# Optimization experiments

Hardware: AMD Instinct MI355X
Metric: run time of the kernel (lower is better)

The kernel has to match this reference:

```python
import jax, jax.numpy as jnp
import numpy as np

B, N, DIM = 1, 32768, 512
H, DH = 8, 64            # heads, dim_head
INNER = H * DH           # 512
L = 64                   # n_cluster = clip(N // (16*16) + 1, 16, 64) = 64 landmarks
ITERS = 6                # pinv_iterations
KS = 33                  # residual_conv_kernel


def setup_inputs() -> dict:
    key = jax.random.key(0)
    k1, k2, k3, k4, k5 = jax.random.split(key, 5)
    x = jax.random.normal(k1, (B, N, DIM), jnp.float32)
    labels = jax.random.randint(k2, (N,), 0, L, jnp.int32)  # kmeans cluster ids (no_grad constants)
    Wqkv = jax.random.normal(k3, (DIM, 3 * INNER), jnp.float32) * 0.02
    Wout = jax.random.normal(k4, (INNER, DIM), jnp.float32) * 0.02
    bout = jnp.zeros((DIM,), jnp.float32)
    res_kernel = jax.random.normal(k5, (H, 1, KS, 1), jnp.float32) * 0.05  # depthwise conv, groups=H
    return dict(x=x, Wqkv=Wqkv, Wout=Wout, bout=bout, res_kernel=res_kernel, labels=labels)


def _pinv(a, iters=ITERS):
    # Moore-Penrose via Newton-Schulz, matching moore_penrose_iter_pinv (global max normalization)
    abs_a = jnp.abs(a)
    z = a.swapaxes(-1, -2) / (abs_a.sum(-1).max() * abs_a.sum(-2).max())
    I = jnp.eye(a.shape[-1], dtype=a.dtype)
    for _ in range(iters):
        az = a @ z
        z = 0.25 * z @ (13.0 * I - az @ (15.0 * I - az @ (7.0 * I - az)))
    return z


def _pool_mean(t, seg):
    # ragged per-cluster mean: t [b,h,n,d], seg [n] sorted cluster ids -> [b,h,L,d]
    b, h, n, d = t.shape
    flat = t.transpose(2, 0, 1, 3).reshape(n, b * h * d)
    sums = jax.ops.segment_sum(flat, seg, num_segments=L)
    counts = jax.ops.segment_sum(jnp.ones((n,), t.dtype), seg, num_segments=L)
    means = sums / jnp.maximum(counts, 1.0)[:, None]
    return means.reshape(L, b, h, d).transpose(1, 2, 0, 3)


def reference(x, Wqkv, Wout, bout, res_kernel, labels):
    # cluster sort / unsort (mirrors x[:, index] ... out[:, index_ori])
    index = jnp.argsort(labels)
    index_ori = jnp.argsort(index)
    seg = labels[index]                      # sorted segment ids
    xp = x[:, index]

    qkv = xp @ Wqkv                          # [b,n,3*inner]
    q, k, v = jnp.split(qkv, 3, axis=-1)
    to_bhnd = lambda t: t.reshape(B, N, H, DH).transpose(0, 2, 1, 3)
    q, k, v = to_bhnd(q), to_bhnd(k), to_bhnd(v)

    ql = _pool_mean(q, seg)                  # [b,h,L,d]
    kl = _pool_mean(k, seg)

    # note: original forward never multiplies by self.scale
    attn1 = jax.nn.softmax(jnp.einsum('bhnd,bhld->bhnl', q, kl), axis=-1)   # [b,h,n,L]
    attn2 = jax.nn.softmax(jnp.einsum('bhid,bhjd->bhij', ql, kl), axis=-1)  # [b,h,L,L]
    attn3 = jax.nn.softmax(jnp.einsum('bhld,bhnd->bhln', ql, k), axis=-1)   # [b,h,L,n]

    out = attn1 @ (_pinv(attn2) @ (attn3 @ v))                              # [b,h,n,d]

    # residual depthwise conv over token axis (Conv2d(h,h,(33,1),groups=h))
    res = jax.lax.conv_general_dilated(
        v, res_kernel, window_strides=(1, 1),
        padding=((KS // 2, KS // 2), (0, 0)),
        dimension_numbers=('NCHW', 'OIHW', 'NCHW'),
        feature_group_count=H)
    out = out + res

    out = out.transpose(0, 2, 1, 3).reshape(B, N, INNER)
    out = out @ Wout + bout
    return out[:, index_ori]
```

## Files before the change

kernel.cpp:

```cpp
#include <hip/hip_runtime.h>
#include <hip/hip_bf16.h>

#define N_TOK 32768
#define DIMC  512
#define NH    8
#define DHD   64
#define NL    64
#define KSZ   33
#define QKVC  1536
#define NCHUNK 64

typedef _Float16 f16;
typedef _Float16 f16x8 __attribute__((ext_vector_type(8)));
typedef _Float16 f16x4 __attribute__((ext_vector_type(4)));
typedef float    f32x4 __attribute__((ext_vector_type(4)));

#define GLOAD_LDS16(gp, lp) \
    __builtin_amdgcn_global_load_lds((const __attribute__((address_space(1))) void*)(gp), \
                                     (__attribute__((address_space(3))) void*)(lp), 16, 0, 0)

__global__ void transpose_k(const float* __restrict__ W, f16* __restrict__ WT, int R, int C) {
    __shared__ float tile[32][33];
    int bx = blockIdx.x * 32, by = blockIdx.y * 32;
    int tx = threadIdx.x, ty = threadIdx.y;
    #pragma unroll
    for (int i = 0; i < 32; i += 8)
        tile[ty + i][tx] = W[(size_t)(by + ty + i) * C + bx + tx];
    __syncthreads();
    #pragma unroll
    for (int i = 0; i < 32; i += 8)
        WT[(size_t)(bx + ty + i) * R + by + tx] = (f16)tile[tx][ty + i];
}

__global__ void hist_k(const int* __restrict__ labels, int* __restrict__ counts) {
    __shared__ int hloc[NL];
    int t = threadIdx.x;
    if (t < NL) hloc[t] = 0;
    __syncthreads();
    int i = blockIdx.x * 256 + t;
    atomicAdd(&hloc[labels[i]], 1);
    __syncthreads();
    if (t < NL) atomicAdd(&counts[t], hloc[t]);
}

__global__ __launch_bounds__(256) void compact_k(const int* __restrict__ labels,
                                                 const int* __restrict__ counts,
                                                 int* __restrict__ indexArr) {
    const int l = blockIdx.x;
    __shared__ int wtot[4];
    __shared__ int s_run;
    int t = threadIdx.x, lane = t & 63, w = t >> 6;
    if (t == 0) {
        int s = 0;
        for (int j = 0; j < l; ++j) s += counts[j];
        s_run = s;
    }
    __syncthreads();
    for (int c0 = 0; c0 < N_TOK; c0 += 256) {
        int ii = c0 + t;
        bool flag = (labels[ii] == l);
        unsigned long long mask = __ballot(flag);
        int before = __popcll(mask & ((1ull << lane) - 1ull));
        if (lane == 0) wtot[w] = __popcll(mask);
        __syncthreads();
        int off = 0;
        #pragma unroll
        for (int ww = 0; ww < 4; ++ww) off += (ww < w) ? wtot[ww] : 0;
        int tot = wtot[0] + wtot[1] + wtot[2] + wtot[3];
        int rb = s_run;
        if (flag) indexArr[rb + off + before] = ii;
        __syncthreads();
        if (t == 0) s_run = rb + tot;
    }
}

__global__ __launch_bounds__(256) void gather_cvt_k(const float4* __restrict__ x4,
                                                    const int* __restrict__ indexArr,
                                                    f16x4* __restrict__ xh4) {
    int t = threadIdx.x;
    int row = blockIdx.x * 2 + (t >> 7);
    int c4 = t & 127;
    int j = indexArr[row];
    float4 v = x4[(size_t)j * 128 + c4];
    f16x4 o = { (f16)v.x, (f16)v.y, (f16)v.z, (f16)v.w };
    xh4[(size_t)row * 128 + c4] = o;
}

template<int BNTOT, bool OUT_F32, int NY>
__global__ __launch_bounds__(512, 4) void gemm_k512(const f16* __restrict__ A, const f16* __restrict__ BT,
                                                    void* __restrict__ Cout, const float* __restrict__ bias,
                                                    const int* __restrict__ scatterIdx) {
    constexpr int K = 512;
    constexpr int NKT = K / 32;
    __shared__ f16 As[3][128 * 32];
    __shared__ f16 Bs[3][256 * 32];
    const int t = threadIdx.x;
    const int orig = blockIdx.x + gridDim.x * blockIdx.y;
    constexpr int NWG = 256 * NY;
    constexpr int CPX = NWG / 8;
    const int lin = (orig & 7) * CPX + (orig >> 3);
    const int mBase = (lin / NY) * 128;
    const int nBase = (lin % NY) * 256;
    const int w = t >> 6, lane = t & 63;
    const int wm = w >> 2, wn = w & 3;
    const int lr = lane & 15, lk = lane >> 4;
    const int kc = (lk ^ ((lr >> 1) & 3)) * 8;
    f32x4 acc[4][4];
    #pragma unroll
    for (int m = 0; m < 4; ++m)
        #pragma unroll
        for (int n = 0; n < 4; ++n) acc[m][n] = (f32x4){0.f, 0.f, 0.f, 0.f};

    auto stage = [&](int buf, int kt) {
        {
            int id = t;
            int row = id >> 2, c = id & 3;
            int cg = c ^ ((row >> 1) & 3);
            GLOAD_LDS16(&A[(size_t)(mBase + row) * K + kt * 32 + cg * 8],
                        &As[buf][(size_t)(w * 64) * 8]);
        }
        #pragma unroll
        for (int r = 0; r < 2; ++r) {
            int id = r * 512 + t;
            int row = id >> 2, c = id & 3;
            int cg = c ^ ((row >> 1) & 3);
            GLOAD_LDS16(&BT[(size_t)(nBase + row) * K + kt * 32 + cg * 8],
                        &Bs[buf][(size_t)(r * 512 + w * 64) * 8]);
        }
    };
    auto compute = [&](int buf) {
        f16x8 af[4], bf[4];
        #pragma unroll
        for (int m = 0; m < 4; ++m)
            af[m] = *(const f16x8*)&As[buf][(wm * 64 + m * 16 + lr) * 32 + kc];
        #pragma unroll
        for (int n = 0; n < 4; ++n)
            bf[n] = *(const f16x8*)&Bs[buf][(wn * 64 + n * 16 + lr) * 32 + kc];
        #pragma unroll
        for (int m = 0; m < 4; ++m)
            #pragma unroll
            for (int n = 0; n < 4; ++n)
                acc[m][n] = __builtin_amdgcn_mfma_f32_16x16x32_f16(bf[n], af[m], acc[m][n], 0, 0, 0);
    };

    stage(0, 0);
    asm volatile("" ::: "memory");
    stage(1, 1);
    for (int kt = 0; kt < NKT; ++kt) {
        if (kt < NKT - 1) {
            asm volatile("s_waitcnt vmcnt(3)" ::: "memory");
        } else {
            asm volatile("s_waitcnt vmcnt(0)" ::: "memory");
        }
        __builtin_amdgcn_s_barrier();
        if (kt + 2 < NKT) stage((kt + 2) % 3, kt + 2);
        compute(kt % 3);
    }

    #pragma unroll
    for (int m = 0; m < 4; ++m) {
        int row = mBase + wm * 64 + m * 16 + lr;
        int srow = OUT_F32 ? scatterIdx[row] : row;
        #pragma unroll
        for (int n = 0; n < 4; ++n) {
            int col = nBase + wn * 64 + n * 16 + lk * 4;
            if constexpr (OUT_F32) {
                float4 bv = *(const float4*)&bias[col];
                float4 sv = make_float4(acc[m][n][0] + bv.x, acc[m][n][1] + bv.y,
                                        acc[m][n][2] + bv.z, acc[m][n][3] + bv.w);
                *(float4*)&((float*)Cout)[(size_t)srow * BNTOT + col] = sv;
            } else {
                f16x4 hv = { (f16)acc[m][n][0], (f16)acc[m][n][1],
                             (f16)acc[m][n][2], (f16)acc[m][n][3] };
                *(f16x4*)&((f16*)Cout)[(size_t)srow * BNTOT + col] = hv;
            }
        }
    }
}

__global__ __launch_bounds__(256) void pool_part_k(const f16* __restrict__ qkvh,
                                                   const int* __restrict__ counts,
                                                   float* __restrict__ psum) {
    int l = blockIdx.x, g = blockIdx.y;
    int t = threadIdx.x;
    int c = t & 127, rg = t >> 7;
    int b0 = 0;
    for (int j = 0; j < l; ++j) b0 += counts[j];
    int cnt = counts[l];
    f32x4 a0 = {0.f,0.f,0.f,0.f}, a1 = {0.f,0.f,0.f,0.f};
    for (int p = g * 2 + rg; p < cnt; p += 8) {
        f16x8 v = *(const f16x8*)&qkvh[(size_t)(b0 + p) * QKVC + c * 8];
        a0[0] += (float)v[0]; a0[1] += (float)v[1]; a0[2] += (float)v[2]; a0[3] += (float)v[3];
        a1[0] += (float)v[4]; a1[1] += (float)v[5]; a1[2] += (float)v[6]; a1[3] += (float)v[7];
    }
    __shared__ f32x4 red[2][128][2];
    red[rg][c][0] = a0; red[rg][c][1] = a1;
    __syncthreads();
    if (t < 128) {
        f32x4 s0 = red[0][t][0] + red[1][t][0];
        f32x4 s1 = red[0][t][1] + red[1][t][1];
        size_t o = ((size_t)g * NL + l) * 1024 + t * 8;
        *(f32x4*)&psum[o] = s0;
        *(f32x4*)&psum[o + 4] = s1;
    }
}

__global__ __launch_bounds__(256) void pool_fin_k(const float* __restrict__ psum,
                                                  const int* __restrict__ counts,
                                                  float* __restrict__ ql, float* __restrict__ kl,
                                                  f16* __restrict__ qlh, f16* __restrict__ klh) {
    int l = blockIdx.x;
    int t = threadIdx.x;
    int bse = t * 4;
    float inv = 1.0f / (float)(counts[l] > 0 ? counts[l] : 1);
    f32x4 s = {0.f,0.f,0.f,0.f};
    #pragma unroll
    for (int g = 0; g < 4; ++g)
        s += *(const f32x4*)&psum[((size_t)g * NL + l) * 1024 + bse];
    s *= inv;
    f16x4 hv = { (f16)s[0], (f16)s[1], (f16)s[2], (f16)s[3] };
    if (bse < 512) {
        int h = bse >> 6, d0 = bse & 63;
        size_t o = ((size_t)(h * 64 + l)) * 64 + d0;
        *(f32x4*)&ql[o] = s;
        *(f16x4*)&qlh[o] = hv;
    } else {
        int bb = bse - 512;
        int h = bb >> 6, d0 = bb & 63;
        size_t o = ((size_t)(h * 64 + l)) * 64 + d0;
        *(f32x4*)&kl[o] = s;
        *(f16x4*)&klh[o] = hv;
    }
}

__global__ __launch_bounds__(256) void attn2_k(const float* __restrict__ ql, const float* __restrict__ kl,
                                               float* __restrict__ a_out, float* __restrict__ mrow,
                                               float* __restrict__ mcol) {
    int h = blockIdx.x;
    __shared__ float qs[64][65], ks[64][65], a[64][65];
    __shared__ float red[64][4];
    __shared__ float rowv[64], colv[64];
    int t = threadIdx.x;
    for (int idx = t; idx < 4096; idx += 256) {
        int r = idx >> 6, c = idx & 63;
        qs[r][c] = ql[h * 4096 + idx];
        ks[r][c] = kl[h * 4096 + idx];
    }
    __syncthreads();
    int i = t >> 2, q4 = t & 3, j0 = q4 * 16;
    float o[16];
    #pragma unroll
    for (int jj = 0; jj < 16; ++jj) o[jj] = 0.f;
    for (int d = 0; d < 64; ++d) {
        float qv = qs[i][d];
        #pragma unroll
        for (int jj = 0; jj < 16; ++jj) o[jj] += qv * ks[j0 + jj][d];
    }
    float pmx = o[0];
    #pragma unroll
    for (int jj = 1; jj < 16; ++jj) pmx = fmaxf(pmx, o[jj]);
    red[i][q4] = pmx;
    __syncthreads();
    float rm = fmaxf(fmaxf(red[i][0], red[i][1]), fmaxf(red[i][2], red[i][3]));
    float psum = 0.f;
    #pragma unroll
    for (int jj = 0; jj < 16; ++jj) { o[jj] = expf(o[jj] - rm); psum += o[jj]; }
    __syncthreads();
    red[i][q4] = psum;
    __syncthreads();
    float rs = red[i][0] + red[i][1] + red[i][2] + red[i][3];
    float inv = 1.0f / rs;
    #pragma unroll
    for (int jj = 0; jj < 16; ++jj) { o[jj] *= inv; a[i][j0 + jj] = o[jj]; }
    __syncthreads();
    for (int idx = t; idx < 4096; idx += 256) a_out[h * 4096 + idx] = a[idx >> 6][idx & 63];
    float rsum = 0.f;
    #pragma unroll
    for (int jj = 0; jj < 16; ++jj) rsum += o[jj];
    __syncthreads();
    red[i][q4] = rsum;
    __syncthreads();
    if (q4 == 0) rowv[i] = red[i][0] + red[i][1] + red[i][2] + red[i][3];
    float csum = 0.f;
    #pragma unroll
    for (int jj = 0; jj < 16; ++jj) csum += a[j0 + jj][i];
    __syncthreads();
    red[i][q4] = csum;
    __syncthreads();
    if (q4 == 0) colv[i] = red[i][0] + red[i][1] + red[i][2] + red[i][3];
    __syncthreads();
    if (t == 0) {
        float mr = rowv[0], mc = colv[0];
        for (int j = 1; j < 64; ++j) { mr = fmaxf(mr, rowv[j]); mc = fmaxf(mc, colv[j]); }
        mrow[h] = mr; mcol[h] = mc;
    }
}

__global__ __launch_bounds__(256) void attn3_pinv_k(const f16* __restrict__ qkvh,
                                                    const f16* __restrict__ qlh,
                                                    float* __restrict__ pm, float* __restrict__ ps,
                                                    float* __restrict__ pacc,
                                                    const float* __restrict__ a_g,
                                                    const float* __restrict__ mrow,
                                                    const float* __restrict__ mcol,
                                                    float* __restrict__ zg) {
    union ShU {
        struct { f16 Qls[64 * 64]; f16 Ks[64 * 64]; f16 vT[64 * 72]; f16 Ps[64 * 72]; float fsh[64]; } a3;
        struct { f16 zRh[64][72], zRl[64][72], cRh[64][72], cRl[64][72],
                 Xh[64][72], Xl[64][72], Yh[64][72], Yl[64][72]; } pv;
    };
    __shared__ ShU sh;
    const int t = threadIdx.x;
    const int w = t >> 6, lane = t & 63;
    const int lr = lane & 15;
    const int h = blockIdx.y;

    if (blockIdx.x == 0) {
        const int lk = lane >> 4;
        f16 (&zRh)[64][72] = sh.pv.zRh; f16 (&zRl)[64][72] = sh.pv.zRl;
        f16 (&cRh)[64][72] = sh.pv.cRh; f16 (&cRl)[64][72] = sh.pv.cRl;
        f16 (&Xh)[64][72]  = sh.pv.Xh;  f16 (&Xl)[64][72]  = sh.pv.Xl;
        f16 (&Yh)[64][72]  = sh.pv.Yh;  f16 (&Yl)[64][72]  = sh.pv.Yl;
        float mr = mrow[0], mc = mcol[0];
        #pragma unroll
        for (int k = 1; k < 8; ++k) { mr = fmaxf(mr, mrow[k]); mc = fmaxf(mc, mcol[k]); }
        const float inv0 = 1.0f / (mr * mc);
        for (int idx = t; idx < 4096; idx += 256) {
            int r = idx >> 6, c = idx & 63;
            float zv = a_g[h * 4096 + idx] * inv0;
            f16 hv = (f16)zv;
            zRh[c][r] = hv; zRl[c][r] = (f16)(zv - (float)hv);
        }
        __syncthreads();

        f32x4 po[4];
        auto product = [&](const f16 (*Lh)[72], const f16 (*Ll)[72],
                           const f16 (*Rh)[72], const f16 (*Rl)[72]) {
            #pragma unroll
            for (int n = 0; n < 4; ++n) po[n] = (f32x4){0.f, 0.f, 0.f, 0.f};
            #pragma unroll
            for (int ck = 0; ck < 2; ++ck) {
                f16x8 axh = *(const f16x8*)&Lh[w * 16 + lr][ck * 32 + lk * 8];
                f16x8 axl = *(const f16x8*)&Ll[w * 16 + lr][ck * 32 + lk * 8];
                #pragma unroll
                for (int n = 0; n < 4; ++n) {
                    f16x8 byh = *(const f16x8*)&Rh[n * 16 + lr][ck * 32 + lk * 8];
                    f16x8 byl = *(const f16x8*)&Rl[n * 16 + lr][ck * 32 + lk * 8];
                    po[n] = __builtin_amdgcn_mfma_f32_16x16x32_f16(byh, axh, po[n], 0, 0, 0);
                    po[n] = __builtin_amdgcn_mfma_f32_16x16x32_f16(byl, axh, po[n], 0, 0, 0);
                    po[n] = __builtin_amdgcn_mfma_f32_16x16x32_f16(byh, axl, po[n], 0, 0, 0);
                }
            }
        };

        for (int it = 0; it < 6; ++it) {
            for (int idx = t; idx < 4096; idx += 256) {
                int r = idx >> 6, c = idx & 63;
                float av = a_g[h * 4096 + idx];
                f16 ah = (f16)av;
                Xh[r][c] = ah; Xl[r][c] = (f16)(av - (float)ah);
                float zv = (float)zRh[r][c] + (float)zRl[r][c];
                f16 zh = (f16)zv;
                Yh[c][r] = zh; Yl[c][r] = (f16)(zv - (float)zh);
            }
            __syncthreads();
            product(Xh, Xl, Yh, Yl);
            __syncthreads();
            #pragma unroll
            for (int n = 0; n < 4; ++n)
                #pragma unroll
                for (int j = 0; j < 4; ++j) {
                    int r = w * 16 + lr, c = n * 16 + lk * 4 + j;
                    float v = po[n][j]; f16 hv = (f16)v; f16 lv = (f16)(v - (float)hv);
                    cRh[r][c] = hv; cRl[r][c] = lv;
                    Xh[c][r] = hv;  Xl[c][r] = lv;
                }
            __syncthreads();
            product(cRh, cRl, Xh, Xl);
            #pragma unroll
            for (int n = 0; n < 4; ++n)
                #pragma unroll
                for (int j = 0; j < 4; ++j) {
                    int r = w * 16 + lr, c = n * 16 + lk * 4 + j;
                    float v = 7.f * ((float)cRh[r][c] + (float)cRl[r][c]) - po[n][j];
                    f16 hv = (f16)v;
                    Yh[c][r] = hv; Yl[c][r] = (f16)(v - (float)hv);
                }
            __syncthreads();
            product(cRh, cRl, Yh, Yl);
            #pragma unroll
            for (int n = 0; n < 4; ++n)
                #pragma unroll
                for (int j = 0; j < 4; ++j) {
                    int r = w * 16 + lr, c = n * 16 + lk * 4 + j;
                    float v = 15.f * ((float)cRh[r][c] + (float)cRl[r][c]) - po[n][j];
                    f16 hv = (f16)v;
                    Xh[c][r] = hv; Xl[c][r] = (f16)(v - (float)hv);
                }
            __syncthreads();
            product(zRh, zRl, Xh, Xl);
            #pragma unroll
            for (int n = 0; n < 4; ++n)
                #pragma unroll
                for (int j = 0; j < 4; ++j) {
                    int r = w * 16 + lr, c = n * 16 + lk * 4 + j;
                    float v = 0.25f * (13.f * ((float)zRh[r][c] + (float)zRl[r][c]) - po[n][j]);
                    f16 hv = (f16)v;
                    zRh[r][c] = hv; zRl[r][c] = (f16)(v - (float)hv);
                }
            __syncthreads();
        }
        for (int idx = t; idx < 4096; idx += 256) {
            int r = idx >> 6, c = idx & 63;
            zg[h * 4096 + idx] = (float)zRh[r][c] + (float)zRl[r][c];
        }
        return;
    }

    const int cx = blockIdx.x - 1;
    const int hi = lane >> 4;
    f16* Qls = sh.a3.Qls;
    f16* Ks  = sh.a3.Ks;
    f16* vT  = sh.a3.vT;
    f16* Ps  = sh.a3.Ps;
    float* fsh = sh.a3.fsh;

    #pragma unroll
    for (int pss = 0; pss < 2; ++pss) {
        int q = pss * 256 + t;
        int r = q >> 3, cs = (q & 7) ^ (r & 7);
        GLOAD_LDS16(&qlh[(size_t)h * 4096 + r * 64 + cs * 8], &Qls[(size_t)(pss * 256 + w * 64) * 8]);
    }
    float m_reg = -1e30f, s_reg = 0.f;
    f32x4 accT[4];
    #pragma unroll
    for (int lf = 0; lf < 4; ++lf) accT[lf] = (f32x4){0.f, 0.f, 0.f, 0.f};

    const int vk8 = t & 7, vnn = t >> 3;

    for (int sub = 0; sub < 8; ++sub) {
        const int n0 = cx * 512 + sub * 64;
        __syncthreads();
        #pragma unroll
        for (int pss = 0; pss < 2; ++pss) {
            int q = pss * 256 + t;
            int r = q >> 3, cs = (q & 7) ^ (r & 7);
            GLOAD_LDS16(&qkvh[(size_t)(n0 + r) * QKVC + 512 + h * 64 + cs * 8],
                        &Ks[(size_t)(pss * 256 + w * 64) * 8]);
        }
        #pragma unroll
        for (int p2 = 0; p2 < 2; ++p2) {
            int n = vnn + 32 * p2;
            f16x8 rv = *(const f16x8*)&qkvh[(size_t)(n0 + n) * QKVC + 1024 + h * 64 + vk8 * 8];
            #pragma unroll
            for (int i = 0; i < 8; ++i) {
                int e = i ^ vk8;
                vT[(vk8 * 8 + e) * 72 + n] = rv[e];
            }
        }
        __syncthreads();
        f32x4 c[4];
        #pragma unroll
        for (int kf = 0; kf < 4; ++kf) c[kf] = (f32x4){0.f, 0.f, 0.f, 0.f};
        const int lq = w * 16 + lr;
        #pragma unroll
        for (int ks = 0; ks < 2; ++ks) {
            f16x8 bf = *(const f16x8*)&Qls[lq * 64 + (((ks * 4 + hi) ^ (lq & 7)) * 8)];
            #pragma unroll
            for (int kf = 0; kf < 4; ++kf) {
                int rn = kf * 16 + lr;
                f16x8 af = *(const f16x8*)&Ks[rn * 64 + (((ks * 4 + hi) ^ (rn & 7)) * 8)];
                c[kf] = __builtin_amdgcn_mfma_f32_16x16x32_f16(af, bf, c[kf], 0, 0, 0);
            }
        }
        float tmax = -1e30f;
        #pragma unroll
        for (int kf = 0; kf < 4; ++kf)
            #pragma unroll
            for (int j = 0; j < 4; ++j) tmax = fmaxf(tmax, c[kf][j]);
        tmax = fmaxf(tmax, __shfl_xor(tmax, 16));
        tmax = fmaxf(tmax, __shfl_xor(tmax, 32));
        float newm = fmaxf(m_reg, tmax);
        float fct = __expf(m_reg - newm);
        float psum = 0.f;
        #pragma unroll
        for (int kf = 0; kf < 4; ++kf) {
            f16x4 pk;
            #pragma unroll
            for (int j = 0; j < 4; ++j) {
                float e = __expf(c[kf][j] - newm);
                psum += e;
                pk[j] = (f16)e;
            }
            *(f16x4*)&Ps[lq * 72 + kf * 16 + hi * 4] = pk;
        }
        psum += __shfl_xor(psum, 16);
        psum += __shfl_xor(psum, 32);
        s_reg = s_reg * fct + psum;
        m_reg = newm;
        if (hi == 0) fsh[lq] = fct;
        __syncthreads();
        #pragma unroll
        for (int lf = 0; lf < 4; ++lf) {
            f32x4 fr = *(const f32x4*)&fsh[lf * 16 + hi * 4];
            accT[lf] *= fr;
        }
        #pragma unroll
        for (int ks = 0; ks < 2; ++ks) {
            f16x8 bf = *(const f16x8*)&vT[(w * 16 + lr) * 72 + ks * 32 + hi * 8];
            #pragma unroll
            for (int lf = 0; lf < 4; ++lf) {
                f16x8 af = *(const f16x8*)&Ps[(lf * 16 + lr) * 72 + ks * 32 + hi * 8];
                accT[lf] = __builtin_amdgcn_mfma_f32_16x16x32_f16(af, bf, accT[lf], 0, 0, 0);
            }
        }
    }
    int part = h * NCHUNK + cx;
    if (hi == 0) {
        pm[part * 64 + w * 16 + lr] = m_reg;
        ps[part * 64 + w * 16 + lr] = s_reg;
    }
    #pragma unroll
    for (int lf = 0; lf < 4; ++lf)
        #pragma unroll
        for (int j = 0; j < 4; ++j)
            pacc[((size_t)part * 64 + (lf * 16 + hi * 4 + j)) * 64 + (w * 16 + lr)] = accT[lf][j];
}

__global__ void attn3_merge_k(const float* __restrict__ pm, const float* __restrict__ ps,
                              const float* __restrict__ pacc, float* __restrict__ T) {
    int l = blockIdx.x, h = blockIdx.y, d = threadIdx.x;
    float m = -1e30f;
    for (int c = 0; c < NCHUNK; ++c) m = fmaxf(m, pm[(h * NCHUNK + c) * 64 + l]);
    float s = 0.f, a = 0.f;
    for (int c = 0; c < NCHUNK; ++c) {
        float wgt = __expf(pm[(h * NCHUNK + c) * 64 + l] - m);
        s += ps[(h * NCHUNK + c) * 64 + l] * wgt;
        a += pacc[((size_t)(h * NCHUNK + c) * 64 + l) * 64 + d] * wgt;
    }
    T[(h * 64 + l) * 64 + d] = a / s;
}

__global__ __launch_bounds__(256) void zmatT_fin_k(const float* __restrict__ zg,
                                                   const float* __restrict__ T,
                                                   f16* __restrict__ MthHi, f16* __restrict__ MthLo) {
    const int h = blockIdx.x;
    __shared__ f16 zFh[64][72], zFl[64][72], tCh[64][72], tCl[64][72];
    const int t = threadIdx.x;
    const int w = t >> 6, lane = t & 63;
    const int lr = lane & 15, lk = lane >> 4;
    for (int idx = t; idx < 4096; idx += 256) {
        int r = idx >> 6, c = idx & 63;
        float zv = zg[h * 4096 + idx]; f16 zh = (f16)zv;
        zFh[r][c] = zh; zFl[r][c] = (f16)(zv - (float)zh);
        float tv = T[h * 4096 + idx]; f16 th = (f16)tv;
        tCh[c][r] = th; tCl[c][r] = (f16)(tv - (float)th);
    }
    __syncthreads();
    f32x4 po[4];
    #pragma unroll
    for (int n = 0; n < 4; ++n) po[n] = (f32x4){0.f, 0.f, 0.f, 0.f};
    #pragma unroll
    for (int ck = 0; ck < 2; ++ck) {
        f16x8 axh = *(const f16x8*)&zFh[w * 16 + lr][ck * 32 + lk * 8];
        f16x8 axl = *(const f16x8*)&zFl[w * 16 + lr][ck * 32 + lk * 8];
        #pragma unroll
        for (int n = 0; n < 4; ++n) {
            f16x8 byh = *(const f16x8*)&tCh[n * 16 + lr][ck * 32 + lk * 8];
            f16x8 byl = *(const f16x8*)&tCl[n * 16 + lr][ck * 32 + lk * 8];
            po[n] = __builtin_amdgcn_mfma_f32_16x16x32_f16(byh, axh, po[n], 0, 0, 0);
            po[n] = __builtin_amdgcn_mfma_f32_16x16x32_f16(byl, axh, po[n], 0, 0, 0);
            po[n] = __builtin_amdgcn_mfma_f32_16x16x32_f16(byh, axl, po[n], 0, 0, 0);
        }
    }
    #pragma unroll
    for (int n = 0; n < 4; ++n)
        #pragma unroll
        for (int j = 0; j < 4; ++j) {
            int r = w * 16 + lr, c = n * 16 + lk * 4 + j;
            float v = po[n][j]; f16 hv = (f16)v;
            MthHi[h * 4096 + c * 64 + r] = hv;
            MthLo[h * 4096 + c * 64 + r] = (f16)(v - (float)hv);
        }
}

__global__ __launch_bounds__(256) void attn1_k(const f16* __restrict__ qkvh, const f16* __restrict__ klh,
                                               const f16* __restrict__ MthHi, const f16* __restrict__ MthLo,
                                               const float* __restrict__ resk, f16* __restrict__ Yh) {
    const int h = blockIdx.y;
    const int p0 = blockIdx.x * 128;
    const int t = threadIdx.x;
    const int w = t >> 6, lane = t & 63;
    const int lr = lane & 15, hi = lane >> 4;
    __shared__ f16 QPs[128][72];
    __shared__ f16 Ks[64][72];
    __shared__ f16 Mhi[64][72];
    __shared__ f16 Mlo[64][72];
    __shared__ f16 vt[160][72];

    #pragma unroll
    for (int i = 0; i < 4; ++i) {
        int id = i * 256 + t, row = id >> 3, c8 = id & 7;
        *(f16x8*)&QPs[row][c8 * 8] = *(const f16x8*)&qkvh[(size_t)(p0 + row) * QKVC + h * 64 + c8 * 8];
    }
    #pragma unroll
    for (int i = 0; i < 2; ++i) {
        int id = i * 256 + t, row = id >> 3, c8 = id & 7;
        *(f16x8*)&Ks[row][c8 * 8]  = *(const f16x8*)&klh[h * 4096 + id * 8];
        *(f16x8*)&Mhi[row][c8 * 8] = *(const f16x8*)&MthHi[h * 4096 + id * 8];
        *(f16x8*)&Mlo[row][c8 * 8] = *(const f16x8*)&MthLo[h * 4096 + id * 8];
    }
    for (int id = t; id < 160 * 8; id += 256) {
        int rr = id >> 3, c8 = id & 7;
        int pg = p0 - 16 + rr;
        int4 v = {0, 0, 0, 0};
        if (pg >= 0 && pg < N_TOK)
            v = *(const int4*)&qkvh[(size_t)pg * QKVC + 1024 + h * 64 + c8 * 8];
        *(int4*)&vt[rr][c8 * 8] = v;
    }
    float wk[KSZ];
    #pragma unroll
    for (int k = 0; k < KSZ; ++k) wk[k] = resk[h * KSZ + k];
    __syncthreads();

    f32x4 c[4][2];
    #pragma unroll
    for (int lf = 0; lf < 4; ++lf)
        #pragma unroll
        for (int nf = 0; nf < 2; ++nf) c[lf][nf] = (f32x4){0.f, 0.f, 0.f, 0.f};
    #pragma unroll
    for (int ks = 0; ks < 2; ++ks) {
        f16x8 af[4], bf[2];
        #pragma unroll
        for (int lf = 0; lf < 4; ++lf) af[lf] = *(const f16x8*)&Ks[lf * 16 + lr][ks * 32 + hi * 8];
        #pragma unroll
        for (int nf = 0; nf < 2; ++nf) bf[nf] = *(const f16x8*)&QPs[w * 32 + nf * 16 + lr][ks * 32 + hi * 8];
        #pragma unroll
        for (int lf = 0; lf < 4; ++lf)
            #pragma unroll
            for (int nf = 0; nf < 2; ++nf)
                c[lf][nf] = __builtin_amdgcn_mfma_f32_16x16x32_f16(af[lf], bf[nf], c[lf][nf], 0, 0, 0);
    }

    #pragma unroll
    for (int nf = 0; nf < 2; ++nf) {
        float m = -1e30f;
        #pragma unroll
        for (int lf = 0; lf < 4; ++lf)
            #pragma unroll
            for (int j = 0; j < 4; ++j) m = fmaxf(m, c[lf][nf][j]);
        m = fmaxf(m, __shfl_xor(m, 16));
        m = fmaxf(m, __shfl_xor(m, 32));
        float s = 0.f;
        #pragma unroll
        for (int lf = 0; lf < 4; ++lf)
            #pragma unroll
            for (int j = 0; j < 4; ++j) { float e = __expf(c[lf][nf][j] - m); c[lf][nf][j] = e; s += e; }
        s += __shfl_xor(s, 16);
        s += __shfl_xor(s, 32);
        float inv = 1.0f / s;
        #pragma unroll
        for (int lf = 0; lf < 4; ++lf) {
            f16x4 pk;
            #pragma unroll
            for (int j = 0; j < 4; ++j) pk[j] = (f16)(c[lf][nf][j] * inv);
            *(f16x4*)&QPs[w * 32 + nf * 16 + lr][lf * 16 + hi * 4] = pk;
        }
    }

    f32x4 o[2][4];
    #pragma unroll
    for (int nf = 0; nf < 2; ++nf)
        #pragma unroll
        for (int df = 0; df < 4; ++df) o[nf][df] = (f32x4){0.f, 0.f, 0.f, 0.f};
    #pragma unroll
    for (int ks = 0; ks < 2; ++ks) {
        f16x8 pa[2], bh[4], bl[4];
        #pragma unroll
        for (int nf = 0; nf < 2; ++nf) pa[nf] = *(const f16x8*)&QPs[w * 32 + nf * 16 + lr][ks * 32 + hi * 8];
        #pragma unroll
        for (int df = 0; df < 4; ++df) {
            bh[df] = *(const f16x8*)&Mhi[df * 16 + lr][ks * 32 + hi * 8];
            bl[df] = *(const f16x8*)&Mlo[df * 16 + lr][ks * 32 + hi * 8];
        }
        #pragma unroll
        for (int nf = 0; nf < 2; ++nf)
            #pragma unroll
            for (int df = 0; df < 4; ++df) {
                o[nf][df] = __builtin_amdgcn_mfma_f32_16x16x32_f16(pa[nf], bh[df], o[nf][df], 0, 0, 0);
                o[nf][df] = __builtin_amdgcn_mfma_f32_16x16x32_f16(pa[nf], bl[df], o[nf][df], 0, 0, 0);
            }
    }

    #pragma unroll
    for (int nf = 0; nf < 2; ++nf)
        #pragma unroll
        for (int df = 0; df < 4; ++df)
            #pragma unroll
            for (int j = 0; j < 4; ++j)
                QPs[w * 32 + nf * 16 + hi * 4 + j][df * 16 + lr] = (f16)(o[nf][df][j]);
    __syncthreads();

    const int d = t & 63, rg = t >> 6;
    #pragma unroll
    for (int hh = 0; hh < 2; ++hh) {
        const int r0 = rg * 32 + hh * 16;
        float col[48];
        #pragma unroll
        for (int j = 0; j < 48; ++j) col[j] = (float)vt[r0 + j][d];
        #pragma unroll
        for (int pp = 0; pp < 16; ++pp) {
            float acc = 0.f;
            #pragma unroll
            for (int k = 0; k < KSZ; ++k) acc += wk[k] * col[pp + k];
            int row = r0 + pp;
            Yh[(size_t)(p0 + row) * 512 + h * 64 + d] = (f16)(acc + (float)QPs[row][d]);
        }
    }
}

extern "C" void kernel_launch(void* const* d_in, const int* in_sizes, int n_in,
                              void* d_out, int out_size, void* d_ws, size_t ws_size,
                              hipStream_t stream) {
    const float* x    = (const float*)d_in[0];
    const float* Wqkv = (const float*)d_in[1];
    const float* Wout = (const float*)d_in[2];
    const float* bout = (const float*)d_in[3];
    const float* resk = (const float*)d_in[4];
    const int*   labels = (const int*)d_in[5];
    float* out = (float*)d_out;

    char* w = (char*)d_ws;
    size_t off = 0;
    auto alloc = [&](size_t bytes) {
        void* p = w + off;
        off += (bytes + 255) & ~(size_t)255;
        return p;
    };
    f16* xh     = (f16*)alloc((size_t)N_TOK * DIMC * 2);
    f16* qkvh   = (f16*)alloc((size_t)N_TOK * QKVC * 2);
    f16* WqkvT  = (f16*)alloc((size_t)QKVC * DIMC * 2);
    f16* WoutT  = (f16*)alloc((size_t)DIMC * DIMC * 2);
    f16* Yh     = (f16*)alloc((size_t)N_TOK * DIMC * 2);
    int* counts = (int*)alloc(NL * 4);
    int* indexA = (int*)alloc((size_t)N_TOK * 4);
    float* ql   = (float*)alloc((size_t)NH * 64 * 64 * 4);
    float* kl   = (float*)alloc((size_t)NH * 64 * 64 * 4);
    f16* qlh    = (f16*)alloc((size_t)NH * 64 * 64 * 2);
    f16* klh    = (f16*)alloc((size_t)NH * 64 * 64 * 2);
    float* a2   = (float*)alloc((size_t)NH * 64 * 64 * 4);
    float* mrow = (float*)alloc(NH * 4);
    float* mcol = (float*)alloc(NH * 4);
    float* Tb   = (float*)alloc((size_t)NH * 64 * 64 * 4);
    float* zg   = (float*)alloc((size_t)NH * 64 * 64 * 4);
    f16* MthHi  = (f16*)alloc((size_t)NH * 64 * 64 * 2);
    f16* MthLo  = (f16*)alloc((size_t)NH * 64 * 64 * 2);
    float* pm   = (float*)alloc((size_t)NH * NCHUNK * 64 * 4);
    float* ps   = (float*)alloc((size_t)NH * NCHUNK * 64 * 4);
    float* pacc = (float*)alloc((size_t)NH * NCHUNK * 64 * 64 * 4);
    float* psum = (float*)alloc((size_t)4 * NL * 1024 * 4);

    hipMemsetAsync(counts, 0, NL * 4, stream);

    hist_k<<<N_TOK / 256, 256, 0, stream>>>(labels, counts);
    compact_k<<<NL, 256, 0, stream>>>(labels, counts, indexA);
    gather_cvt_k<<<N_TOK / 2, 256, 0, stream>>>((const float4*)x, indexA, (f16x4*)xh);
    transpose_k<<<dim3(QKVC / 32, DIMC / 32), dim3(32, 8), 0, stream>>>(Wqkv, WqkvT, DIMC, QKVC);
    transpose_k<<<dim3(DIMC / 32, DIMC / 32), dim3(32, 8), 0, stream>>>(Wout, WoutT, DIMC, DIMC);
    gemm_k512<QKVC, false, 6><<<dim3(N_TOK / 128, QKVC / 256), 512, 0, stream>>>(xh, WqkvT, qkvh, nullptr, nullptr);
    pool_part_k<<<dim3(NL, 4), 256, 0, stream>>>(qkvh, counts, psum);
    pool_fin_k<<<NL, 256, 0, stream>>>(psum, counts, ql, kl, qlh, klh);
    attn2_k<<<NH, 256, 0, stream>>>(ql, kl, a2, mrow, mcol);
    attn3_pinv_k<<<dim3(NCHUNK + 1, NH), 256, 0, stream>>>(qkvh, qlh, pm, ps, pacc, a2, mrow, mcol, zg);
    attn3_merge_k<<<dim3(NL, NH), 64, 0, stream>>>(pm, ps, pacc, Tb);
    zmatT_fin_k<<<NH, 256, 0, stream>>>(zg, Tb, MthHi, MthLo);
    attn1_k<<<dim3(N_TOK / 128, NH), 256, 0, stream>>>(qkvh, klh, MthHi, MthLo, resk, Yh);
    gemm_k512<DIMC, true, 2><<<dim3(N_TOK / 128, DIMC / 256), 512, 0, stream>>>(Yh, WoutT, out, bout, indexA);
}
```

Before: 338.3 us.

## Parallelize cluster compaction with per-chunk histograms and vectorize residual conv

Replaces the serial per-label compaction (64 blocks, each scanning all 32768 labels over 128 barrier-synchronized steps) with a chunked counting sort: per-chunk histograms, a single-block scan producing per-chunk bases and global bases, then a parallel placement pass using in-block rank counting. This keeps the index order stable and lets pool_part_k reuse the precomputed global bases. The residual conv in attn1_k now handles two channels per thread with half2 loads and stores, which raises per-thread register use.

```diff
diff --git a/kernel.cpp b/kernel.cpp
--- a/kernel.cpp
+++ b/kernel.cpp
@@ -13,6 +13,7 @@
 typedef _Float16 f16;
 typedef _Float16 f16x8 __attribute__((ext_vector_type(8)));
 typedef _Float16 f16x4 __attribute__((ext_vector_type(4)));
+typedef _Float16 f16x2 __attribute__((ext_vector_type(2)));
 typedef float    f32x4 __attribute__((ext_vector_type(4)));
 
 #define GLOAD_LDS16(gp, lp) \
@@ -32,46 +33,47 @@
         WT[(size_t)(bx + ty + i) * R + by + tx] = (f16)tile[tx][ty + i];
 }
 
-__global__ void hist_k(const int* __restrict__ labels, int* __restrict__ counts) {
+__global__ __launch_bounds__(256) void hist_chunk_k(const int* __restrict__ labels,
+                                                    int* __restrict__ counts,
+                                                    int* __restrict__ chunkCnt) {
     __shared__ int hloc[NL];
-    int t = threadIdx.x;
+    int t = threadIdx.x, c = blockIdx.x;
     if (t < NL) hloc[t] = 0;
     __syncthreads();
-    int i = blockIdx.x * 256 + t;
-    atomicAdd(&hloc[labels[i]], 1);
-    __syncthreads();
-    if (t < NL) atomicAdd(&counts[t], hloc[t]);
-}
-
-__global__ __launch_bounds__(256) void compact_k(const int* __restrict__ labels,
-                                                 const int* __restrict__ counts,
-                                                 int* __restrict__ indexArr) {
-    const int l = blockIdx.x;
-    __shared__ int wtot[4];
-    __shared__ int s_run;
-    int t = threadIdx.x, lane = t & 63, w = t >> 6;
-    if (t == 0) {
-        int s = 0;
-        for (int j = 0; j < l; ++j) s += counts[j];
-        s_run = s;
-    }
-    __syncthreads();
-    for (int c0 = 0; c0 < N_TOK; c0 += 256) {
-        int ii = c0 + t;
-        bool flag = (labels[ii] == l);
-        unsigned long long mask = __ballot(flag);
-        int before = __popcll(mask & ((1ull << lane) - 1ull));
-        if (lane == 0) wtot[w] = __popcll(mask);
-        __syncthreads();
-        int off = 0;
-        #pragma unroll
-        for (int ww = 0; ww < 4; ++ww) off += (ww < w) ? wtot[ww] : 0;
-        int tot = wtot[0] + wtot[1] + wtot[2] + wtot[3];
-        int rb = s_run;
-        if (flag) indexArr[rb + off + before] = ii;
-        __syncthreads();
-        if (t == 0) s_run = rb + tot;
-    }
+    atomicAdd(&hloc[labels[c * 256 + t]], 1);
+    __syncthreads();
+    if (t < NL) {
+        chunkCnt[c * NL + t] = hloc[t];
+        atomicAdd(&counts[t], hloc[t]);
+    }
+}
+
+__global__ void scan_all_k(const int* __restrict__ chunkCnt, const int* __restrict__ counts,
+                           int* __restrict__ baseC, int* __restrict__ baseG) {
+    int l = threadIdx.x;
+    int gb = 0;
+    for (int j = 0; j < l; ++j) gb += counts[j];
+    baseG[l] = gb;
+    int run = gb;
+    for (int c = 0; c < 128; ++c) {
+        baseC[c * NL + l] = run;
+        run += chunkCnt[c * NL + l];
+    }
+}
+
+__global__ __launch_bounds__(256) void place_k(const int* __restrict__ labels,
+                                               const int* __restrict__ baseC,
+                                               int* __restrict__ indexArr) {
+    __shared__ int labs[256];
+    int t = threadIdx.x, c = blockIdx.x;
+    int ii = c * 256 + t;
+    int lab = labels[ii];
+    labs[t] = lab;
+    __syncthreads();
+    int rank = 0;
+    for (int j = 0; j < 256; ++j)
+        rank += (j < t && labs[j] == lab) ? 1 : 0;
+    indexArr[baseC[c * NL + lab] + rank] = ii;
 }
 
 __global__ __launch_bounds__(256) void gather_cvt_k(const float4* __restrict__ x4,
@@ -179,13 +181,13 @@
 }
 
 __global__ __launch_bounds__(256) void pool_part_k(const f16* __restrict__ qkvh,
+                                                   const int* __restrict__ baseG,
                                                    const int* __restrict__ counts,
                                                    float* __restrict__ psum) {
     int l = blockIdx.x, g = blockIdx.y;
     int t = threadIdx.x;
     int c = t & 127, rg = t >> 7;
-    int b0 = 0;
-    for (int j = 0; j < l; ++j) b0 += counts[j];
+    int b0 = baseG[l];
     int cnt = counts[l];
     f32x4 a0 = {0.f,0.f,0.f,0.f}, a1 = {0.f,0.f,0.f,0.f};
     for (int p = g * 2 + rg; p < cnt; p += 8) {
@@ -701,21 +703,25 @@
                 QPs[w * 32 + nf * 16 + hi * 4 + j][df * 16 + lr] = (f16)(o[nf][df][j]);
     __syncthreads();
 
-    const int d = t & 63, rg = t >> 6;
-    #pragma unroll
-    for (int hh = 0; hh < 2; ++hh) {
-        const int r0 = rg * 32 + hh * 16;
-        float col[48];
-        #pragma unroll
-        for (int j = 0; j < 48; ++j) col[j] = (float)vt[r0 + j][d];
-        #pragma unroll
-        for (int pp = 0; pp < 16; ++pp) {
-            float acc = 0.f;
-            #pragma unroll
-            for (int k = 0; k < KSZ; ++k) acc += wk[k] * col[pp + k];
-            int row = r0 + pp;
-            Yh[(size_t)(p0 + row) * 512 + h * 64 + d] = (f16)(acc + (float)QPs[row][d]);
-        }
+    const int d2 = t & 31, rg8 = t >> 5;
+    const int r0 = rg8 * 16;
+    float c0[48], c1[48];
+    #pragma unroll
+    for (int j = 0; j < 48; ++j) {
+        f16x2 v = *(const f16x2*)&vt[r0 + j][d2 * 2];
+        c0[j] = (float)v[0]; c1[j] = (float)v[1];
+    }
+    #pragma unroll
+    for (int pp = 0; pp < 16; ++pp) {
+        float a0 = 0.f, a1 = 0.f;
+        #pragma unroll
+        for (int k = 0; k < KSZ; ++k) { a0 += wk[k] * c0[pp + k]; a1 += wk[k] * c1[pp + k]; }
+        int row = r0 + pp;
+        f16x2 qv = *(const f16x2*)&QPs[row][d2 * 2];
+        f16x2 ov;
+        ov[0] = (f16)(a0 + (float)qv[0]);
+        ov[1] = (f16)(a1 + (float)qv[1]);
+        *(f16x2*)&Yh[(size_t)(p0 + row) * 512 + h * 64 + d2 * 2] = ov;
     }
 }
 
@@ -743,6 +749,9 @@
     f16* WoutT  = (f16*)alloc((size_t)DIMC * DIMC * 2);
     f16* Yh     = (f16*)alloc((size_t)N_TOK * DIMC * 2);
     int* counts = (int*)alloc(NL * 4);
+    int* chunkCnt = (int*)alloc((size_t)128 * NL * 4);
+    int* baseC  = (int*)alloc((size_t)128 * NL * 4);
+    int* baseG  = (int*)alloc(NL * 4);
     int* indexA = (int*)alloc((size_t)N_TOK * 4);
     float* ql   = (float*)alloc((size_t)NH * 64 * 64 * 4);
     float* kl   = (float*)alloc((size_t)NH * 64 * 64 * 4);
@@ -762,13 +771,14 @@
 
     hipMemsetAsync(counts, 0, NL * 4, stream);
 
-    hist_k<<<N_TOK / 256, 256, 0, stream>>>(labels, counts);
-    compact_k<<<NL, 256, 0, stream>>>(labels, counts, indexA);
+    hist_chunk_k<<<128, 256, 0, stream>>>(labels, counts, chunkCnt);
+    scan_all_k<<<1, 64, 0, stream>>>(chunkCnt, counts, baseC, baseG);
+    place_k<<<128, 256, 0, stream>>>(labels, baseC, indexA);
     gather_cvt_k<<<N_TOK / 2, 256, 0, stream>>>((const float4*)x, indexA, (f16x4*)xh);
     transpose_k<<<dim3(QKVC / 32, DIMC / 32), dim3(32, 8), 0, stream>>>(Wqkv, WqkvT, DIMC, QKVC);
     transpose_k<<<dim3(DIMC / 32, DIMC / 32), dim3(32, 8), 0, stream>>>(Wout, WoutT, DIMC, DIMC);
     gemm_k512<QKVC, false, 6><<<dim3(N_TOK / 128, QKVC / 256), 512, 0, stream>>>(xh, WqkvT, qkvh, nullptr, nullptr);
-    pool_part_k<<<dim3(NL, 4), 256, 0, stream>>>(qkvh, counts, psum);
+    pool_part_k<<<dim3(NL, 4), 256, 0, stream>>>(qkvh, baseG, counts, psum);
     pool_fin_k<<<NL, 256, 0, stream>>>(psum, counts, ql, kl, qlh, klh);
     attn2_k<<<NH, 256, 0, stream>>>(ql, kl, a2, mrow, mcol);
     attn3_pinv_k<<<dim3(NCHUNK + 1, NH), 256, 0, stream>>>(qkvh, qlh, pm, ps, pacc, a2, mrow, mcol, zg);
```

Result: faster. 297.4 us (median of 3 runs) (-12.1%).
